# Performance work log

Measured on AMD Instinct MI355X. Metric: run time of the kernel, lower is better.

Reference implementation:

```python
import jax, jax.numpy as jnp
import numpy as np

N, D = 100000, 64        # num nodes, node feature dim
E, DE = 1600000, 64      # num edges, edge feature dim
MSG_H, MSG_OUT = 128, 64 # message MLP hidden sizes (activate_final=True)
NODE_H = 128             # node MLP hidden; final size = D (residual)
LN_EPS = 1e-5


def setup_inputs() -> dict:
    key = jax.random.key(0)
    ks = jax.random.split(key, 10)
    def glorot(k, shape):
        fan_in = shape[0]
        return jax.random.normal(k, shape, jnp.float32) / jnp.sqrt(jnp.float32(fan_in))
    return {
        "nodes": jax.random.normal(ks[0], (N, D), jnp.float32),
        "edges": jax.random.normal(ks[1], (E, DE), jnp.float32),
        "senders": jax.random.randint(ks[2], (E,), 0, N, jnp.int32),
        "receivers": jax.random.randint(ks[3], (E,), 0, N, jnp.int32),
        "msg_W1": glorot(ks[4], (2 * D + DE, MSG_H)),
        "msg_b1": jnp.zeros((MSG_H,), jnp.float32),
        "msg_W2": glorot(ks[5], (MSG_H, MSG_OUT)),
        "msg_b2": jnp.zeros((MSG_OUT,), jnp.float32),
        "node_W1": glorot(ks[6], (D + MSG_OUT, NODE_H)),
        "node_b1": jnp.zeros((NODE_H,), jnp.float32),
        "node_W2": glorot(ks[7], (NODE_H, D)),
        "node_b2": jnp.zeros((D,), jnp.float32),
        "ln_scale": jnp.ones((D,), jnp.float32),
        "ln_offset": jnp.zeros((D,), jnp.float32),
    }


def reference(nodes, edges, senders, receivers,
              msg_W1, msg_b1, msg_W2, msg_b2,
              node_W1, node_b1, node_W2, node_b2,
              ln_scale, ln_offset):
    # --- message MLP (activate_final=True) over concat(sender, receiver, edge)
    x = jnp.concatenate([nodes[senders], nodes[receivers], edges], axis=-1)  # [E, 2D+DE]
    h = jax.nn.relu(x @ msg_W1 + msg_b1)
    messages = jax.nn.relu(h @ msg_W2 + msg_b2)  # [E, MSG_OUT]
    # --- aggregate messages at receivers
    agg = jax.ops.segment_sum(messages, receivers, num_segments=nodes.shape[0])  # [N, MSG_OUT]
    # --- node update MLP (no final activation), sizes [NODE_H, D] due to residual
    y = jnp.concatenate([nodes, agg], axis=-1)  # [N, D+MSG_OUT]
    y = jax.nn.relu(y @ node_W1 + node_b1)
    y = y @ node_W2 + node_b2  # [N, D]
    # --- layer norm over last axis with scale + offset
    mean = jnp.mean(y, axis=-1, keepdims=True)
    var = jnp.var(y, axis=-1, keepdims=True)
    y = (y - mean) * jax.lax.rsqrt(var + LN_EPS) * ln_scale + ln_offset
    # --- residual connection
    return nodes + y
```

## Files before the change

### kernel.cpp

```cpp
#include <hip/hip_runtime.h>

typedef short bf16x8 __attribute__((ext_vector_type(8)));
typedef float floatx4 __attribute__((ext_vector_type(4)));
typedef unsigned short u16x4 __attribute__((ext_vector_type(4)));
typedef unsigned short u16x8 __attribute__((ext_vector_type(8)));

__device__ __forceinline__ unsigned short f2bf(float f) {
  union { float f; unsigned int u; } v;
  v.f = f;
  unsigned int u = v.u + (0x7FFFu + ((v.u >> 16) & 1u));
  return (unsigned short)(u >> 16);
}

__device__ __forceinline__ bf16x8 pack8(float4 a, float4 b) {
  u16x8 h;
  h[0] = f2bf(a.x); h[1] = f2bf(a.y); h[2] = f2bf(a.z); h[3] = f2bf(a.w);
  h[4] = f2bf(b.x); h[5] = f2bf(b.y); h[6] = f2bf(b.z); h[7] = f2bf(b.w);
  union { u16x8 u; bf16x8 s; } cv; cv.u = h; return cv.s;
}

__global__ __launch_bounds__(256) void prep_weights(
    const float* __restrict__ mW1, const float* __restrict__ mW2,
    const float* __restrict__ nW1, const float* __restrict__ nW2,
    unsigned short* __restrict__ W1f, unsigned short* __restrict__ W2f,
    unsigned short* __restrict__ NW1f, unsigned short* __restrict__ NW2f) {
  int idx = blockIdx.x * 256 + threadIdx.x;
  if (idx < 24576) {
    int j = idx & 7, n = (idx >> 3) & 127, g = idx >> 10;
    W1f[idx] = f2bf(mW1[(g * 8 + j) * 128 + n]);
  } else if (idx < 32768) {
    int t = idx - 24576;
    int j = t & 7, n = (t >> 3) & 63, g = t >> 9;
    W2f[t] = f2bf(mW2[(g * 8 + j) * 64 + n]);
  } else if (idx < 49152) {
    int t = idx - 32768;
    int j = t & 7, n = (t >> 3) & 127, g = t >> 10;
    NW1f[t] = f2bf(nW1[(g * 8 + j) * 128 + n]);
  } else if (idx < 57344) {
    int t = idx - 49152;
    int j = t & 7, n = (t >> 3) & 63, g = t >> 9;
    NW2f[t] = f2bf(nW2[(g * 8 + j) * 64 + n]);
  }
}

__global__ __launch_bounds__(256) void conv_nodes(
    const float* __restrict__ nodes, unsigned short* __restrict__ nodes_bf, int total4) {
  int i = (blockIdx.x * 256 + threadIdx.x) * 4;
  if (i < total4) {
    float4 v = *(const float4*)(nodes + i);
    u16x4 h; h[0] = f2bf(v.x); h[1] = f2bf(v.y); h[2] = f2bf(v.z); h[3] = f2bf(v.w);
    *(u16x4*)(nodes_bf + i) = h;
  }
}

__global__ __launch_bounds__(256, 4) void edge_kernel(
    const float* __restrict__ edges, const unsigned short* __restrict__ nodes_bf,
    const int* __restrict__ senders, const int* __restrict__ receivers,
    const unsigned short* __restrict__ W1f, const unsigned short* __restrict__ W2f,
    const float* __restrict__ b1, const float* __restrict__ b2,
    float* agg, int E) {
  __shared__ unsigned short Hf[16 * 128 * 8];

  const int tid = threadIdx.x;
  const int e0 = blockIdx.x * 128;
  const int w = tid >> 6, lane = tid & 63;
  const int col = lane & 15, quad = lane >> 4;
  const int wm = w & 1, wn = w >> 1;

  int srow[4], sndi[4], rcvi[4];
#pragma unroll
  for (int mt = 0; mt < 4; ++mt) {
    int r = e0 + wm * 64 + mt * 16 + col;
    srow[mt] = r < E ? r : E - 1;
  }
#pragma unroll
  for (int mt = 0; mt < 4; ++mt) { sndi[mt] = senders[srow[mt]]; rcvi[mt] = receivers[srow[mt]]; }

  floatx4 z4 = {0.f, 0.f, 0.f, 0.f};
  floatx4 acc1[4][4];
#pragma unroll
  for (int mt = 0; mt < 4; ++mt)
#pragma unroll
    for (int nt = 0; nt < 4; ++nt) acc1[mt][nt] = z4;

#pragma unroll
  for (int ks = 0; ks < 4; ++ks) {
    bf16x8 a[4], b[4];
#pragma unroll
    for (int mt = 0; mt < 4; ++mt) {
      int nd = (ks < 2) ? sndi[mt] : rcvi[mt];
      a[mt] = *(const bf16x8*)&nodes_bf[(size_t)nd * 64 + (ks & 1) * 32 + quad * 8];
    }
#pragma unroll
    for (int nt = 0; nt < 4; ++nt)
      b[nt] = *(const bf16x8*)&W1f[ks * 4096 + quad * 1024 + (wn * 64 + nt * 16 + col) * 8];
#pragma unroll
    for (int mt = 0; mt < 4; ++mt)
#pragma unroll
      for (int nt = 0; nt < 4; ++nt)
        acc1[mt][nt] = __builtin_amdgcn_mfma_f32_16x16x32_bf16(a[mt], b[nt], acc1[mt][nt], 0, 0, 0);
  }
#pragma unroll
  for (int ks = 4; ks < 6; ++ks) {
    bf16x8 a[4], b[4];
#pragma unroll
    for (int mt = 0; mt < 4; ++mt) {
      const float* p = edges + (size_t)srow[mt] * 64 + (ks - 4) * 32 + quad * 8;
      float4 v0 = *(const float4*)p;
      float4 v1 = *(const float4*)(p + 4);
      a[mt] = pack8(v0, v1);
    }
#pragma unroll
    for (int nt = 0; nt < 4; ++nt)
      b[nt] = *(const bf16x8*)&W1f[ks * 4096 + quad * 1024 + (wn * 64 + nt * 16 + col) * 8];
#pragma unroll
    for (int mt = 0; mt < 4; ++mt)
#pragma unroll
      for (int nt = 0; nt < 4; ++nt)
        acc1[mt][nt] = __builtin_amdgcn_mfma_f32_16x16x32_bf16(a[mt], b[nt], acc1[mt][nt], 0, 0, 0);
  }

#pragma unroll
  for (int nt = 0; nt < 4; ++nt) {
    float bias = b1[wn * 64 + nt * 16 + col];
    int c = wn * 64 + nt * 16 + col;
    unsigned short* dst = &Hf[((c >> 3) * 128) * 8 + (c & 7)];
#pragma unroll
    for (int mt = 0; mt < 4; ++mt)
#pragma unroll
      for (int r = 0; r < 4; ++r) {
        float v = acc1[mt][nt][r] + bias;
        v = v > 0.f ? v : 0.f;
        int row = wm * 64 + mt * 16 + quad * 4 + r;
        dst[row * 8] = f2bf(v);
      }
  }
  __syncthreads();

  floatx4 acc2[4][2];
#pragma unroll
  for (int mt = 0; mt < 4; ++mt) { acc2[mt][0] = z4; acc2[mt][1] = z4; }

#pragma unroll
  for (int ks = 0; ks < 4; ++ks) {
    bf16x8 a[4], b[2];
#pragma unroll
    for (int mt = 0; mt < 4; ++mt)
      a[mt] = *(const bf16x8*)&Hf[((ks * 4 + quad) * 128 + (wm * 64 + mt * 16 + col)) * 8];
#pragma unroll
    for (int nt = 0; nt < 2; ++nt)
      b[nt] = *(const bf16x8*)&W2f[ks * 2048 + quad * 512 + (wn * 32 + nt * 16 + col) * 8];
#pragma unroll
    for (int mt = 0; mt < 4; ++mt)
#pragma unroll
      for (int nt = 0; nt < 2; ++nt)
        acc2[mt][nt] = __builtin_amdgcn_mfma_f32_16x16x32_bf16(a[mt], b[nt], acc2[mt][nt], 0, 0, 0);
  }

  float bs0 = b2[wn * 32 + col];
  float bs1 = b2[wn * 32 + 16 + col];
#pragma unroll
  for (int mt = 0; mt < 4; ++mt)
#pragma unroll
    for (int r = 0; r < 4; ++r) {
      int er = e0 + wm * 64 + mt * 16 + quad * 4 + r;
      if (er < E) {
        int rv = receivers[er];
        float v0 = acc2[mt][0][r] + bs0; v0 = v0 > 0.f ? v0 : 0.f;
        float v1 = acc2[mt][1][r] + bs1; v1 = v1 > 0.f ? v1 : 0.f;
        atomicAdd(&agg[(size_t)rv * 64 + wn * 32 + col], v0);
        atomicAdd(&agg[(size_t)rv * 64 + wn * 32 + 16 + col], v1);
      }
    }
}

__global__ __launch_bounds__(256, 3) void node_kernel(
    const float* __restrict__ nodes, const unsigned short* __restrict__ nodes_bf,
    const float* agg,
    const unsigned short* __restrict__ W1f, const unsigned short* __restrict__ W2f,
    const float* __restrict__ b1, const float* __restrict__ b2,
    const float* __restrict__ ln_s, const float* __restrict__ ln_o,
    float* out, int N) {
  __shared__ unsigned short Hf[16 * 128 * 8];
  __shared__ float Ls1[128][2];
  __shared__ float Ls2[128][2];

  const int tid = threadIdx.x;
  const int n0 = blockIdx.x * 128;
  const int w = tid >> 6, lane = tid & 63;
  const int col = lane & 15, quad = lane >> 4;
  const int wm = w & 1, wn = w >> 1;

  int arow[4];
#pragma unroll
  for (int mt = 0; mt < 4; ++mt) {
    int r = n0 + wm * 64 + mt * 16 + col;
    arow[mt] = r < N ? r : N - 1;
  }

  floatx4 z4 = {0.f, 0.f, 0.f, 0.f};
  floatx4 acc1[4][4];
#pragma unroll
  for (int mt = 0; mt < 4; ++mt)
#pragma unroll
    for (int nt = 0; nt < 4; ++nt) acc1[mt][nt] = z4;

#pragma unroll
  for (int ks = 0; ks < 2; ++ks) {
    bf16x8 a[4], b[4];
#pragma unroll
    for (int mt = 0; mt < 4; ++mt)
      a[mt] = *(const bf16x8*)&nodes_bf[(size_t)arow[mt] * 64 + ks * 32 + quad * 8];
#pragma unroll
    for (int nt = 0; nt < 4; ++nt)
      b[nt] = *(const bf16x8*)&W1f[ks * 4096 + quad * 1024 + (wn * 64 + nt * 16 + col) * 8];
#pragma unroll
    for (int mt = 0; mt < 4; ++mt)
#pragma unroll
      for (int nt = 0; nt < 4; ++nt)
        acc1[mt][nt] = __builtin_amdgcn_mfma_f32_16x16x32_bf16(a[mt], b[nt], acc1[mt][nt], 0, 0, 0);
  }
#pragma unroll
  for (int ks = 2; ks < 4; ++ks) {
    bf16x8 a[4], b[4];
#pragma unroll
    for (int mt = 0; mt < 4; ++mt) {
      const float* p = agg + (size_t)arow[mt] * 64 + (ks - 2) * 32 + quad * 8;
      float4 v0 = *(const float4*)p;
      float4 v1 = *(const float4*)(p + 4);
      a[mt] = pack8(v0, v1);
    }
#pragma unroll
    for (int nt = 0; nt < 4; ++nt)
      b[nt] = *(const bf16x8*)&W1f[ks * 4096 + quad * 1024 + (wn * 64 + nt * 16 + col) * 8];
#pragma unroll
    for (int mt = 0; mt < 4; ++mt)
#pragma unroll
      for (int nt = 0; nt < 4; ++nt)
        acc1[mt][nt] = __builtin_amdgcn_mfma_f32_16x16x32_bf16(a[mt], b[nt], acc1[mt][nt], 0, 0, 0);
  }

#pragma unroll
  for (int nt = 0; nt < 4; ++nt) {
    float bias = b1[wn * 64 + nt * 16 + col];
    int c = wn * 64 + nt * 16 + col;
    unsigned short* dst = &Hf[((c >> 3) * 128) * 8 + (c & 7)];
#pragma unroll
    for (int mt = 0; mt < 4; ++mt)
#pragma unroll
      for (int r = 0; r < 4; ++r) {
        float v = acc1[mt][nt][r] + bias;
        v = v > 0.f ? v : 0.f;
        int row = wm * 64 + mt * 16 + quad * 4 + r;
        dst[row * 8] = f2bf(v);
      }
  }
  __syncthreads();

  floatx4 acc2[4][2];
#pragma unroll
  for (int mt = 0; mt < 4; ++mt) { acc2[mt][0] = z4; acc2[mt][1] = z4; }

#pragma unroll
  for (int ks = 0; ks < 4; ++ks) {
    bf16x8 a[4], b[2];
#pragma unroll
    for (int mt = 0; mt < 4; ++mt)
      a[mt] = *(const bf16x8*)&Hf[((ks * 4 + quad) * 128 + (wm * 64 + mt * 16 + col)) * 8];
#pragma unroll
    for (int nt = 0; nt < 2; ++nt)
      b[nt] = *(const bf16x8*)&W2f[ks * 2048 + quad * 512 + (wn * 32 + nt * 16 + col) * 8];
#pragma unroll
    for (int mt = 0; mt < 4; ++mt)
#pragma unroll
      for (int nt = 0; nt < 2; ++nt)
        acc2[mt][nt] = __builtin_amdgcn_mfma_f32_16x16x32_bf16(a[mt], b[nt], acc2[mt][nt], 0, 0, 0);
  }

  float y[4][2][4];
  float bs0 = b2[wn * 32 + col];
  float bs1 = b2[wn * 32 + 16 + col];
#pragma unroll
  for (int mt = 0; mt < 4; ++mt)
#pragma unroll
    for (int r = 0; r < 4; ++r) {
      y[mt][0][r] = acc2[mt][0][r] + bs0;
      y[mt][1][r] = acc2[mt][1][r] + bs1;
    }

#pragma unroll
  for (int mt = 0; mt < 4; ++mt)
#pragma unroll
    for (int r = 0; r < 4; ++r) {
      float p1 = y[mt][0][r] + y[mt][1][r];
      float p2 = y[mt][0][r] * y[mt][0][r] + y[mt][1][r] * y[mt][1][r];
#pragma unroll
      for (int m = 1; m <= 8; m <<= 1) {
        p1 += __shfl_xor(p1, m);
        p2 += __shfl_xor(p2, m);
      }
      if (col == 0) {
        int row = wm * 64 + mt * 16 + quad * 4 + r;
        Ls1[row][wn] = p1;
        Ls2[row][wn] = p2;
      }
    }
  __syncthreads();

  float lsv0 = ln_s[wn * 32 + col], lsv1 = ln_s[wn * 32 + 16 + col];
  float lov0 = ln_o[wn * 32 + col], lov1 = ln_o[wn * 32 + 16 + col];
#pragma unroll
  for (int mt = 0; mt < 4; ++mt)
#pragma unroll
    for (int r = 0; r < 4; ++r) {
      int row = wm * 64 + mt * 16 + quad * 4 + r;
      int gi = n0 + row;
      float s1 = Ls1[row][0] + Ls1[row][1];
      float s2 = Ls2[row][0] + Ls2[row][1];
      float mean = s1 * (1.f / 64.f);
      float var = s2 * (1.f / 64.f) - mean * mean;
      float rstd = rsqrtf(var + 1e-5f);
      if (gi < N) {
        int j0 = wn * 32 + col;
        float o0 = (y[mt][0][r] - mean) * rstd * lsv0 + lov0 + nodes[(size_t)gi * 64 + j0];
        float o1 = (y[mt][1][r] - mean) * rstd * lsv1 + lov1 + nodes[(size_t)gi * 64 + j0 + 16];
        out[(size_t)gi * 64 + j0] = o0;
        out[(size_t)gi * 64 + j0 + 16] = o1;
      }
    }
}

extern "C" void kernel_launch(void* const* d_in, const int* in_sizes, int n_in,
                              void* d_out, int out_size, void* d_ws, size_t ws_size,
                              hipStream_t stream) {
  const float* nodes     = (const float*)d_in[0];
  const float* edges     = (const float*)d_in[1];
  const int*   senders   = (const int*)d_in[2];
  const int*   receivers = (const int*)d_in[3];
  const float* msg_W1    = (const float*)d_in[4];
  const float* msg_b1    = (const float*)d_in[5];
  const float* msg_W2    = (const float*)d_in[6];
  const float* msg_b2    = (const float*)d_in[7];
  const float* node_W1   = (const float*)d_in[8];
  const float* node_b1   = (const float*)d_in[9];
  const float* node_W2   = (const float*)d_in[10];
  const float* node_b2   = (const float*)d_in[11];
  const float* ln_scale  = (const float*)d_in[12];
  const float* ln_offset = (const float*)d_in[13];

  const int N = in_sizes[0] / 64;
  const int E = in_sizes[2];

  unsigned short* W1f  = (unsigned short*)d_ws;
  unsigned short* W2f  = W1f + 24576;
  unsigned short* NW1f = W2f + 8192;
  unsigned short* NW2f = NW1f + 16384;
  unsigned short* nodes_bf = NW2f + 8192;

  float* agg = (float*)d_out;

  hipMemsetAsync(d_out, 0, (size_t)out_size * sizeof(float), stream);
  prep_weights<<<224, 256, 0, stream>>>(msg_W1, msg_W2, node_W1, node_W2, W1f, W2f, NW1f, NW2f);
  conv_nodes<<<(N * 64 + 1023) / 1024, 256, 0, stream>>>(nodes, nodes_bf, N * 64);
  edge_kernel<<<(E + 127) / 128, 256, 0, stream>>>(edges, nodes_bf, senders, receivers,
                                                   W1f, W2f, msg_b1, msg_b2, agg, E);
  node_kernel<<<(N + 127) / 128, 256, 0, stream>>>(nodes, nodes_bf, agg, NW1f, NW2f,
                                                   node_b1, node_b2, ln_scale, ln_offset,
                                                   (float*)d_out, N);
}
```

Before: 992.8 us.

## Sort edges by receiver and pre-reduce messages in-block before atomic adds

Builds a counting-sort permutation of edges by receiver (histogram, scan, scatter) each call. The edge kernel then processes edges in receiver order, stages the messages in shared memory, and run-length combines consecutive rows with the same receiver, so it issues far fewer global float atomics. The cost is several extra kernel launches, random gathers of the edge features through the permutation, and bf16 rounding of messages before accumulation. The node kernel also shares one shared-memory buffer across phases and raises its occupancy hint.

```diff
diff --git a/kernel.cpp b/kernel.cpp
--- a/kernel.cpp
+++ b/kernel.cpp
@@ -10,6 +10,12 @@
   v.f = f;
   unsigned int u = v.u + (0x7FFFu + ((v.u >> 16) & 1u));
   return (unsigned short)(u >> 16);
+}
+
+__device__ __forceinline__ float bf2f(unsigned short h) {
+  union { unsigned int u; float f; } v;
+  v.u = ((unsigned int)h) << 16;
+  return v.f;
 }
 
 __device__ __forceinline__ bf16x8 pack8(float4 a, float4 b) {
@@ -53,6 +59,202 @@
   }
 }
 
+__global__ __launch_bounds__(256) void hist_kernel(
+    const int* __restrict__ recv, int* cnt, int E) {
+  int e = blockIdx.x * 256 + threadIdx.x;
+  if (e < E) atomicAdd(&cnt[recv[e]], 1);
+}
+
+__global__ __launch_bounds__(1024) void scan_blocks(
+    const int* __restrict__ cnt, int* __restrict__ cur, int* __restrict__ blk, int N) {
+  __shared__ int s[1024];
+  int t = threadIdx.x, i = blockIdx.x * 1024 + t;
+  int x = (i < N) ? cnt[i] : 0;
+  s[t] = x;
+  __syncthreads();
+#pragma unroll
+  for (int off = 1; off < 1024; off <<= 1) {
+    int v = (t >= off) ? s[t - off] : 0;
+    __syncthreads();
+    s[t] += v;
+    __syncthreads();
+  }
+  if (i < N) cur[i] = s[t] - x;
+  if (t == 1023) blk[blockIdx.x] = s[t];
+}
+
+__global__ __launch_bounds__(128) void scan_spine(int* blk, int nb) {
+  __shared__ int s[128];
+  int t = threadIdx.x;
+  if (nb <= 128) {
+    if (t < nb) s[t] = blk[t];
+    __syncthreads();
+    if (t == 0) { int run = 0; for (int j = 0; j < nb; ++j) { int v = s[j]; s[j] = run; run += v; } }
+    __syncthreads();
+    if (t < nb) blk[t] = s[t];
+  } else {
+    if (t == 0) { int run = 0; for (int j = 0; j < nb; ++j) { int v = blk[j]; blk[j] = run; run += v; } }
+  }
+}
+
+__global__ __launch_bounds__(1024) void scan_add(
+    int* __restrict__ cur, const int* __restrict__ blk, int N) {
+  int i = blockIdx.x * 1024 + threadIdx.x;
+  if (i < N) cur[i] += blk[blockIdx.x];
+}
+
+__global__ __launch_bounds__(256) void scatter_kernel(
+    const int* __restrict__ recv, int* cur, int* __restrict__ eid, int E) {
+  int e = blockIdx.x * 256 + threadIdx.x;
+  if (e < E) { int p = atomicAdd(&cur[recv[e]], 1); eid[p] = e; }
+}
+
+__global__ __launch_bounds__(256, 4) void edge_kernel_csr(
+    const float* __restrict__ edges, const unsigned short* __restrict__ nodes_bf,
+    const int* __restrict__ senders, const int* __restrict__ receivers,
+    const int* __restrict__ eid,
+    const unsigned short* __restrict__ W1f, const unsigned short* __restrict__ W2f,
+    const float* __restrict__ b1, const float* __restrict__ b2,
+    float* agg, int E) {
+  __shared__ __align__(16) unsigned char smem[32768];
+  unsigned short* Hf = (unsigned short*)smem;
+  unsigned short* Ms = (unsigned short*)smem;
+  int* rcvRow = (int*)(smem + 16384);
+
+  const int tid = threadIdx.x;
+  const int e0 = blockIdx.x * 128;
+  const int w = tid >> 6, lane = tid & 63;
+  const int col = lane & 15, quad = lane >> 4;
+  const int wm = w & 1, wn = w >> 1;
+
+  int eidv[4], sndi[4], rcvi[4];
+#pragma unroll
+  for (int mt = 0; mt < 4; ++mt) {
+    int p = e0 + wm * 64 + mt * 16 + col;
+    p = p < E ? p : E - 1;
+    eidv[mt] = eid[p];
+  }
+#pragma unroll
+  for (int mt = 0; mt < 4; ++mt) { sndi[mt] = senders[eidv[mt]]; rcvi[mt] = receivers[eidv[mt]]; }
+
+  floatx4 z4 = {0.f, 0.f, 0.f, 0.f};
+  floatx4 acc1[4][4];
+#pragma unroll
+  for (int mt = 0; mt < 4; ++mt)
+#pragma unroll
+    for (int nt = 0; nt < 4; ++nt) acc1[mt][nt] = z4;
+
+#pragma unroll
+  for (int ks = 0; ks < 4; ++ks) {
+    bf16x8 a[4], b[4];
+#pragma unroll
+    for (int mt = 0; mt < 4; ++mt) {
+      int nd = (ks < 2) ? sndi[mt] : rcvi[mt];
+      a[mt] = *(const bf16x8*)&nodes_bf[(size_t)nd * 64 + (ks & 1) * 32 + quad * 8];
+    }
+#pragma unroll
+    for (int nt = 0; nt < 4; ++nt)
+      b[nt] = *(const bf16x8*)&W1f[ks * 4096 + quad * 1024 + (wn * 64 + nt * 16 + col) * 8];
+#pragma unroll
+    for (int mt = 0; mt < 4; ++mt)
+#pragma unroll
+      for (int nt = 0; nt < 4; ++nt)
+        acc1[mt][nt] = __builtin_amdgcn_mfma_f32_16x16x32_bf16(a[mt], b[nt], acc1[mt][nt], 0, 0, 0);
+  }
+#pragma unroll
+  for (int ks = 4; ks < 6; ++ks) {
+    bf16x8 a[4], b[4];
+#pragma unroll
+    for (int mt = 0; mt < 4; ++mt) {
+      const float* p = edges + (size_t)eidv[mt] * 64 + (ks - 4) * 32 + quad * 8;
+      float4 v0 = *(const float4*)p;
+      float4 v1 = *(const float4*)(p + 4);
+      a[mt] = pack8(v0, v1);
+    }
+#pragma unroll
+    for (int nt = 0; nt < 4; ++nt)
+      b[nt] = *(const bf16x8*)&W1f[ks * 4096 + quad * 1024 + (wn * 64 + nt * 16 + col) * 8];
+#pragma unroll
+    for (int mt = 0; mt < 4; ++mt)
+#pragma unroll
+      for (int nt = 0; nt < 4; ++nt)
+        acc1[mt][nt] = __builtin_amdgcn_mfma_f32_16x16x32_bf16(a[mt], b[nt], acc1[mt][nt], 0, 0, 0);
+  }
+
+#pragma unroll
+  for (int nt = 0; nt < 4; ++nt) {
+    float bias = b1[wn * 64 + nt * 16 + col];
+    int c = wn * 64 + nt * 16 + col;
+    unsigned short* dst = &Hf[((c >> 3) * 128) * 8 + (c & 7)];
+#pragma unroll
+    for (int mt = 0; mt < 4; ++mt)
+#pragma unroll
+      for (int r = 0; r < 4; ++r) {
+        float v = acc1[mt][nt][r] + bias;
+        v = v > 0.f ? v : 0.f;
+        int row = wm * 64 + mt * 16 + quad * 4 + r;
+        dst[row * 8] = f2bf(v);
+      }
+  }
+  __syncthreads();
+
+  floatx4 acc2[4][2];
+#pragma unroll
+  for (int mt = 0; mt < 4; ++mt) { acc2[mt][0] = z4; acc2[mt][1] = z4; }
+
+#pragma unroll
+  for (int ks = 0; ks < 4; ++ks) {
+    bf16x8 a[4], b[2];
+#pragma unroll
+    for (int mt = 0; mt < 4; ++mt)
+      a[mt] = *(const bf16x8*)&Hf[((ks * 4 + quad) * 128 + (wm * 64 + mt * 16 + col)) * 8];
+#pragma unroll
+    for (int nt = 0; nt < 2; ++nt)
+      b[nt] = *(const bf16x8*)&W2f[ks * 2048 + quad * 512 + (wn * 32 + nt * 16 + col) * 8];
+#pragma unroll
+    for (int mt = 0; mt < 4; ++mt)
+#pragma unroll
+      for (int nt = 0; nt < 2; ++nt)
+        acc2[mt][nt] = __builtin_amdgcn_mfma_f32_16x16x32_bf16(a[mt], b[nt], acc2[mt][nt], 0, 0, 0);
+  }
+  __syncthreads();
+
+  if (tid < 128) {
+    int p = e0 + tid;
+    rcvRow[tid] = (p < E) ? receivers[eid[p]] : -1;
+  }
+  float bs0 = b2[wn * 32 + col];
+  float bs1 = b2[wn * 32 + 16 + col];
+#pragma unroll
+  for (int mt = 0; mt < 4; ++mt)
+#pragma unroll
+    for (int r = 0; r < 4; ++r) {
+      int row = wm * 64 + mt * 16 + quad * 4 + r;
+      float v0 = acc2[mt][0][r] + bs0; v0 = v0 > 0.f ? v0 : 0.f;
+      float v1 = acc2[mt][1][r] + bs1; v1 = v1 > 0.f ? v1 : 0.f;
+      Ms[row * 64 + wn * 32 + col] = f2bf(v0);
+      Ms[row * 64 + wn * 32 + 16 + col] = f2bf(v1);
+    }
+  __syncthreads();
+
+  {
+    int g = tid >> 6, c = tid & 63;
+    float acc = 0.f; int prev = -1;
+#pragma unroll 8
+    for (int i = 0; i < 32; ++i) {
+      int row = g * 32 + i;
+      int rv = rcvRow[row];
+      float v = bf2f(Ms[row * 64 + c]);
+      if (rv != prev) {
+        if (prev >= 0) atomicAdd(&agg[(size_t)prev * 64 + c], acc);
+        prev = rv; acc = 0.f;
+      }
+      if (rv >= 0) acc += v;
+    }
+    if (prev >= 0) atomicAdd(&agg[(size_t)prev * 64 + c], acc);
+  }
+}
+
 __global__ __launch_bounds__(256, 4) void edge_kernel(
     const float* __restrict__ edges, const unsigned short* __restrict__ nodes_bf,
     const int* __restrict__ senders, const int* __restrict__ receivers,
@@ -174,16 +376,17 @@
     }
 }
 
-__global__ __launch_bounds__(256, 3) void node_kernel(
+__global__ __launch_bounds__(256, 4) void node_kernel(
     const float* __restrict__ nodes, const unsigned short* __restrict__ nodes_bf,
     const float* agg,
     const unsigned short* __restrict__ W1f, const unsigned short* __restrict__ W2f,
     const float* __restrict__ b1, const float* __restrict__ b2,
     const float* __restrict__ ln_s, const float* __restrict__ ln_o,
     float* out, int N) {
-  __shared__ unsigned short Hf[16 * 128 * 8];
-  __shared__ float Ls1[128][2];
-  __shared__ float Ls2[128][2];
+  __shared__ __align__(16) unsigned char smem[32768];
+  unsigned short* Hf = (unsigned short*)smem;
+  float (*Ls1)[2] = (float(*)[2])smem;
+  float (*Ls2)[2] = (float(*)[2])(smem + 1024);
 
   const int tid = threadIdx.x;
   const int n0 = blockIdx.x * 128;
@@ -276,6 +479,7 @@
       for (int nt = 0; nt < 2; ++nt)
         acc2[mt][nt] = __builtin_amdgcn_mfma_f32_16x16x32_bf16(a[mt], b[nt], acc2[mt][nt], 0, 0, 0);
   }
+  __syncthreads();
 
   float y[4][2][4];
   float bs0 = b2[wn * 32 + col];
@@ -357,13 +561,34 @@
   unsigned short* NW2f = NW1f + 16384;
   unsigned short* nodes_bf = NW2f + 8192;
 
+  size_t base_bytes = 114688 + (size_t)N * 128;
+  int* cnt = (int*)((char*)d_ws + base_bytes);
+  int* cur = cnt + N;
+  int* blk = cur + N;
+  int* eid = blk + 1024;
+  size_t need = base_bytes + (size_t)N * 8 + 4096 + (size_t)E * 4;
+
   float* agg = (float*)d_out;
 
   hipMemsetAsync(d_out, 0, (size_t)out_size * sizeof(float), stream);
   prep_weights<<<224, 256, 0, stream>>>(msg_W1, msg_W2, node_W1, node_W2, W1f, W2f, NW1f, NW2f);
   conv_nodes<<<(N * 64 + 1023) / 1024, 256, 0, stream>>>(nodes, nodes_bf, N * 64);
-  edge_kernel<<<(E + 127) / 128, 256, 0, stream>>>(edges, nodes_bf, senders, receivers,
-                                                   W1f, W2f, msg_b1, msg_b2, agg, E);
+
+  if (ws_size >= need) {
+    int nb = (N + 1023) / 1024;
+    hipMemsetAsync(cnt, 0, (size_t)N * sizeof(int), stream);
+    hist_kernel<<<(E + 255) / 256, 256, 0, stream>>>(receivers, cnt, E);
+    scan_blocks<<<nb, 1024, 0, stream>>>(cnt, cur, blk, N);
+    scan_spine<<<1, 128, 0, stream>>>(blk, nb);
+    scan_add<<<nb, 1024, 0, stream>>>(cur, blk, N);
+    scatter_kernel<<<(E + 255) / 256, 256, 0, stream>>>(receivers, cur, eid, E);
+    edge_kernel_csr<<<(E + 127) / 128, 256, 0, stream>>>(edges, nodes_bf, senders, receivers,
+                                                         eid, W1f, W2f, msg_b1, msg_b2, agg, E);
+  } else {
+    edge_kernel<<<(E + 127) / 128, 256, 0, stream>>>(edges, nodes_bf, senders, receivers,
+                                                     W1f, W2f, msg_b1, msg_b2, agg, E);
+  }
+
   node_kernel<<<(N + 127) / 128, 256, 0, stream>>>(nodes, nodes_bf, agg, NW1f, NW2f,
                                                    node_b1, node_b2, ln_scale, ln_offset,
                                                    (float*)d_out, N);
```

After: 1.054 ms. 6.2% more time.
